# Performance work log

Measured on AMD Instinct MI355X. Metric: run time of the kernel, lower is better.

Reference implementation:

```python
import jax, jax.numpy as jnp
import numpy as np
from jax import lax

EPS = 1e-20
BN_EPS = 1e-5
ATTN_SCALE = 2.8284271247461903  # sqrt(d_l=8)
NS = (32, 32, 32, 10)
DS = (8, 8, 8, 16)


def squash(x):
    # Efficient-CapsNet squash: (1 - 1/(exp(||x||)+eps)) * x/(||x||+eps)
    norm = jnp.linalg.norm(x, axis=-1, keepdims=True)
    return (1.0 - 1.0 / (jnp.exp(norm) + EPS)) * (x / (norm + EPS))


def conv2d(x, w, b, stride, groups=1):
    y = lax.conv_general_dilated(
        x, w, window_strides=(stride, stride), padding='VALID',
        dimension_numbers=('NCHW', 'OIHW', 'NCHW'),
        feature_group_count=groups)
    return y + b[None, :, None, None]


def bn(x, g, b, m, v):
    inv = g / jnp.sqrt(v + BN_EPS)
    return x * inv[None, :, None, None] + (b - m * inv)[None, :, None, None]


def fccaps(U_l, W):
    # U_l: (b, n_l, d_l), W: (n_l, n_h, d_l, d_h)
    U_hat = jnp.einsum('bij,ikjl->bikl', U_l, W)          # (b, n_l, n_h, d_h)
    A = jnp.einsum('bikl,bhkl->bhik', U_hat, U_hat)        # (b, n_l, n_l, n_h)
    A_sum = jnp.sum(A, axis=-2)                            # (b, n_l, n_h)
    C = jax.nn.softmax(A_sum / ATTN_SCALE, axis=-1)        # (b, n_l, n_h)
    U_h = jnp.einsum('bikl,bik->bkl', U_hat, C)            # (b, n_h, d_h)
    return squash(U_h)


def setup_inputs() -> dict:
    key = jax.random.key(0)
    ks = jax.random.split(key, 8)
    B = 512
    x = jax.random.normal(ks[0], (B, 1, 39, 39), dtype=jnp.float32)
    conv1_w = jax.random.normal(ks[1], (128, 1, 3, 3), jnp.float32) * 0.2
    conv1_b = jnp.zeros((128,), jnp.float32)
    conv2_w = jax.random.normal(ks[2], (256, 128, 3, 3), jnp.float32) * 0.04
    conv2_b = jnp.zeros((256,), jnp.float32)
    conv3_w = jax.random.normal(ks[3], (256, 1, 9, 9), jnp.float32) * 0.1  # depthwise
    conv3_b = jnp.zeros((256,), jnp.float32)
    bn1_g = jnp.ones((128,), jnp.float32); bn1_b = jnp.zeros((128,), jnp.float32)
    bn1_m = jnp.zeros((128,), jnp.float32); bn1_v = jnp.ones((128,), jnp.float32)
    bn2_g = jnp.ones((256,), jnp.float32); bn2_b = jnp.zeros((256,), jnp.float32)
    bn2_m = jnp.zeros((256,), jnp.float32); bn2_v = jnp.ones((256,), jnp.float32)
    # capsule weights, kaiming-ish scale sqrt(2/fan_in) with fan_in = n_h*d_l*d_h
    def caps_w(k, n_l, n_h, d_l, d_h):
        std = np.sqrt(2.0 / (n_h * d_l * d_h))
        return jax.random.normal(k, (n_l, n_h, d_l, d_h), jnp.float32) * std
    W1 = caps_w(ks[4], NS[0], NS[1], DS[0], DS[1])
    W2 = caps_w(ks[5], NS[1], NS[2], DS[1], DS[2])
    W3 = caps_w(ks[6], NS[2], NS[3], DS[2], DS[3])
    return dict(x=x, conv1_w=conv1_w, conv1_b=conv1_b,
                bn1_g=bn1_g, bn1_b=bn1_b, bn1_m=bn1_m, bn1_v=bn1_v,
                conv2_w=conv2_w, conv2_b=conv2_b,
                bn2_g=bn2_g, bn2_b=bn2_b, bn2_m=bn2_m, bn2_v=bn2_v,
                conv3_w=conv3_w, conv3_b=conv3_b, W1=W1, W2=W2, W3=W3)


def reference(x, conv1_w, conv1_b, bn1_g, bn1_b, bn1_m, bn1_v,
              conv2_w, conv2_b, bn2_g, bn2_b, bn2_m, bn2_v,
              conv3_w, conv3_b, W1, W2, W3):
    h = jax.nn.relu(bn(conv2d(x, conv1_w, conv1_b, 2), bn1_g, bn1_b, bn1_m, bn1_v))
    h = jax.nn.relu(bn(conv2d(h, conv2_w, conv2_b, 2), bn2_g, bn2_b, bn2_m, bn2_v))
    h = conv2d(h, conv3_w, conv3_b, 1, groups=256)        # (B, 256, 1, 1)
    u = h.reshape(h.shape[0], NS[0], DS[0])                # (B, 32, 8)
    u = squash(u)
    for W in (W1, W2, W3):
        u = fccaps(u, W)
    return u  # (B, 10, 16)
```

## Files before the change

kernel.cpp:

```cpp
#include <hip/hip_runtime.h>


typedef __attribute__((ext_vector_type(8))) short short8;
typedef __attribute__((ext_vector_type(4))) float f32x4;

__device__ __forceinline__ ushort f2bf(float x) {
    uint u = __float_as_uint(x);
    return (ushort)((u + 0x7FFFu + ((u >> 16) & 1u)) >> 16);
}
__device__ __forceinline__ void bfsplit(float x, ushort& h, ushort& l) {
    h = f2bf(x);
    float hf = __uint_as_float(((uint)h) << 16);
    l = f2bf(x - hf);
}

__global__ __launch_bounds__(256) void k_prep(
    const float* __restrict__ w2, uint* __restrict__ Bt,
    const float* __restrict__ w3, float* __restrict__ w3T,
    const float* __restrict__ W1, const float* __restrict__ W2,
    const float* __restrict__ W3, float* __restrict__ Wr1,
    float* __restrict__ Wr2, float* __restrict__ Wr3,
    const float* __restrict__ c1b, const float* __restrict__ g1,
    const float* __restrict__ b1, const float* __restrict__ m1,
    const float* __restrict__ v1, float2* __restrict__ sc1) {
    __shared__ __align__(16) float wbuf[64 * 288];
    const int b = blockIdx.x, t = threadIdx.x;
    if (b < 144) {
        const int sidx = b >> 2, coq = b & 3;
        const int chunk = sidx / 9, tap = sidx - chunk * 9;
        const int co0 = coq * 64;
        for (int idx = t; idx < 4608; idx += 256) {
            const int n = idx / 72, q = idx - n * 72;
            ((float4*)wbuf)[n * 72 + q] =
                *(const float4*)(w2 + (size_t)(co0 + n) * 1152 + chunk * 288 + q * 4);
        }
        __syncthreads();
        const int n = t & 63, dg = (t >> 6) * 4;
        const int cot = coq >> 1, nn = ((coq & 1) * 64) + n;
        uint* dst = Bt + (size_t)(sidx * 2 + cot) * 4096;
#pragma unroll
        for (int dd = 0; dd < 4; ++dd) {
            const int d = dg + dd;
            const float x = wbuf[n * 288 + (2 * d) * 9 + tap];
            const float y = wbuf[n * 288 + (2 * d + 1) * 9 + tap];
            ushort xh, xl, yh, yl;
            bfsplit(x, xh, xl);
            bfsplit(y, yh, yl);
            dst[nn * 16 + d]        = (uint)xh | ((uint)yh << 16);
            dst[2048 + nn * 16 + d] = (uint)xl | ((uint)yl << 16);
        }
    } else if (b < 225) {
        const int p = b - 144;
        w3T[p * 256 + t] = w3[t * 81 + p];
    } else if (b < 321) {
        const int bb = b - 225;
        const int layer = bb >> 5, blk = bb & 31;
        const float* src = layer == 0 ? W1 : (layer == 1 ? W2 : W3);
        float* dst = layer == 0 ? Wr1 : (layer == 1 ? Wr2 : Wr3);
        const int d_h = (layer == 2) ? 16 : 8;
        const int total = (layer == 2) ? 5120 : 8192;
        for (int idx = blk * 256 + t; idx < 8 * total; idx += 32 * 256) {
            const int j = idx / total, e = idx - j * total;
            const int ik = e / d_h, l = e - ik * d_h;
            dst[idx] = src[(ik * 8 + j) * d_h + l];
        }
    } else {
        if (t < 128) {
            const float inv = g1[t] * rsqrtf(v1[t] + 1e-5f);
            sc1[t] = make_float2(inv, c1b[t] * inv + b1[t] - m1[t] * inv);
        }
    }
}

__global__ __launch_bounds__(512, 4) void k_conv2(
    const float* __restrict__ x, const float* __restrict__ w1,
    const float2* __restrict__ sc1, const uint* __restrict__ Bt,
    const float* __restrict__ g,
    const float* __restrict__ bb, const float* __restrict__ bm,
    const float* __restrict__ bv, const float* __restrict__ bias,
    const float* __restrict__ w3T, float* __restrict__ Uws) {
    __shared__ __align__(16) uint raw[11552];
    __shared__ __align__(16) float xs[1560];
    __shared__ float ured[256];
    const int t = threadIdx.x;
    const int lane = t & 63, wave = t >> 6;
    const int ln15 = lane & 15, lq = lane >> 4;
    const int wm = (wave >> 2) * 48;
    const int wn = (wave & 3) * 64;
    const int cot_w = (wave & 3) >> 1;
    const int bi = blockIdx.x;

    const float* xb = x + (size_t)bi * 1521;
    for (int i = t; i < 1521; i += 512) {
        const int y = i / 39, xc = i - y * 39;
        xs[y * 40 + xc] = xb[i];
    }

    const int qc = t & 15, ol = qc >> 2, qo = (qc & 3) * 2, pg = t >> 4;

    int PE[3], PO[3];
#pragma unroll
    for (int i = 0; i < 3; ++i) {
        const int m = wm + i * 16 + ln15;
        const int p = m < 81 ? m : 80;
        const int oh = p / 9, ow = p - oh * 9;
        PE[i] = lq * 760 + oh * 80 + ow * 4;
        PO[i] = 3040 + lq * 684 + oh * 72 + ow * 4;
    }
    int BRDg[4];
#pragma unroll
    for (int j = 0; j < 4; ++j) {
        const int n = ((wn & 64) + j * 16 + ln15);
        BRDg[j] = n * 16 + lq * 4;
    }

    f32x4 acc[3][4] = {};

#pragma unroll
    for (int c = 0; c < 4; ++c) {
        const int o_g = c * 32 + qc * 2;
        float wr[18];
        {
            const float2* wp = reinterpret_cast<const float2*>(w1 + o_g * 9);
#pragma unroll
            for (int q = 0; q < 9; ++q) {
                const float2 wv = wp[q];
                wr[q * 2] = wv.x; wr[q * 2 + 1] = wv.y;
            }
        }
        float2 ssv[2];
        ssv[0] = sc1[o_g];
        ssv[1] = sc1[o_g + 1];

        __syncthreads();

        {
            ushort* rawu = (ushort*)raw;
            for (int p = pg; p < 361; p += 32) {
                const int y = p / 19, xq = p - y * 19;
                const int b2 = y * 80 + xq * 2;
                const float2 x01 = *(const float2*)(xs + b2);
                const float  x2v = xs[b2 + 2];
                const float2 x34 = *(const float2*)(xs + b2 + 40);
                const float  x5v = xs[b2 + 42];
                const float2 x67 = *(const float2*)(xs + b2 + 80);
                const float  x8v = xs[b2 + 82];
                uint hw, lw;
                {
                    uint hv[2], lv[2];
#pragma unroll
                    for (int jj = 0; jj < 2; ++jj) {
                        const float a = x01.x * wr[jj * 9 + 0] + x01.y * wr[jj * 9 + 1] +
                                        x2v   * wr[jj * 9 + 2] + x34.x * wr[jj * 9 + 3] +
                                        x34.y * wr[jj * 9 + 4] + x5v   * wr[jj * 9 + 5] +
                                        x67.x * wr[jj * 9 + 6] + x67.y * wr[jj * 9 + 7] +
                                        x8v   * wr[jj * 9 + 8];
                        const float v = fmaxf(fmaf(a, ssv[jj].x, ssv[jj].y), 0.0f);
                        const uint u = __float_as_uint(v);
                        hv[jj] = u >> 16;
                        const float d = v - __uint_as_float(u & 0xFFFF0000u);
                        lv[jj] = __float_as_uint(d) >> 16;
                    }
                    hw = hv[0] | (hv[1] << 16);
                    lw = lv[0] | (lv[1] << 16);
                }
                int ad;
                if ((xq & 1) == 0) {
                    ad = ol * 1520 + (y * 10 + (xq >> 1)) * 8 + qo;
                } else {
                    ad = 6080 + ol * 1368 + (y * 9 + (xq >> 1)) * 8 + qo;
                }
                *(uint*)(rawu + ad)         = hw;
                *(uint*)(rawu + 11552 + ad) = lw;
            }
        }
        __syncthreads();

#pragma unroll
        for (int tap = 0; tap < 9; ++tap) {
            const int s = c * 9 + tap;
            const int kh = tap / 3, kw = tap - kh * 3;
            const int odd = kw & 1;
            const int sE = kh * 40 + (kw >> 1) * 4;
            const int sO = kh * 36;
            short8 a_h[3], a_l[3];
#pragma unroll
            for (int i = 0; i < 3; ++i) {
                const int addr = odd ? (PO[i] + sO) : (PE[i] + sE);
                a_h[i] = *reinterpret_cast<const short8*>(raw + addr);
                a_l[i] = *reinterpret_cast<const short8*>(raw + addr + 5776);
            }
            const uint* bp = Bt + (size_t)(s * 2 + cot_w) * 4096;
#pragma unroll
            for (int jh = 0; jh < 2; ++jh) {
                uint4 Bc[4];
#pragma unroll
                for (int j2 = 0; j2 < 2; ++j2) {
                    Bc[j2]     = *(const uint4*)(bp + BRDg[jh * 2 + j2]);
                    Bc[2 + j2] = *(const uint4*)(bp + 2048 + BRDg[jh * 2 + j2]);
                }
                short8 bh[2], bl[2];
#pragma unroll
                for (int j2 = 0; j2 < 2; ++j2) {
                    bh[j2] = __builtin_bit_cast(short8, Bc[j2]);
                    bl[j2] = __builtin_bit_cast(short8, Bc[2 + j2]);
                }
#pragma unroll
                for (int i = 0; i < 3; ++i)
#pragma unroll
                    for (int j2 = 0; j2 < 2; ++j2)
                        acc[i][jh * 2 + j2] = __builtin_amdgcn_mfma_f32_16x16x32_bf16(
                            a_h[i], bh[j2], acc[i][jh * 2 + j2], 0, 0, 0);
#pragma unroll
                for (int i = 0; i < 3; ++i)
#pragma unroll
                    for (int j2 = 0; j2 < 2; ++j2)
                        acc[i][jh * 2 + j2] = __builtin_amdgcn_mfma_f32_16x16x32_bf16(
                            a_h[i], bl[j2], acc[i][jh * 2 + j2], 0, 0, 0);
#pragma unroll
                for (int i = 0; i < 3; ++i)
#pragma unroll
                    for (int j2 = 0; j2 < 2; ++j2)
                        acc[i][jh * 2 + j2] = __builtin_amdgcn_mfma_f32_16x16x32_bf16(
                            a_l[i], bh[j2], acc[i][jh * 2 + j2], 0, 0, 0);
            }
        }
    }

    float scj[4], shj[4];
#pragma unroll
    for (int j = 0; j < 4; ++j) {
        const int co = wn + j * 16 + ln15;
        const float inv = g[co] * rsqrtf(bv[co] + 1e-5f);
        scj[j] = inv;
        shj[j] = bias[co] * inv + bb[co] - bm[co] * inv;
    }
    float usum[4] = {0.f, 0.f, 0.f, 0.f};
#pragma unroll
    for (int i = 0; i < 3; ++i)
#pragma unroll
        for (int r = 0; r < 4; ++r) {
            const int m = wm + i * 16 + lq * 4 + r;
            if (m < 81) {
                const float* wrow = w3T + m * 256;
#pragma unroll
                for (int j = 0; j < 4; ++j) {
                    const int col = wn + j * 16 + ln15;
                    const float v = fmaxf(fmaf(acc[i][j][r], scj[j], shj[j]), 0.0f);
                    usum[j] = fmaf(v, wrow[col], usum[j]);
                }
            }
        }
#pragma unroll
    for (int j = 0; j < 4; ++j) {
        usum[j] += __shfl_xor(usum[j], 16);
        usum[j] += __shfl_xor(usum[j], 32);
    }
    if (lq == 0 && wm == 0) {
#pragma unroll
        for (int j = 0; j < 4; ++j) ured[wn + j * 16 + ln15] = usum[j];
    }
    __syncthreads();
    if (lq == 0 && wm == 48) {
#pragma unroll
        for (int j = 0; j < 4; ++j) {
            const int col = wn + j * 16 + ln15;
            Uws[(size_t)bi * 256 + col] = usum[j] + ured[col];
        }
    }
}

__device__ __forceinline__ void fccaps_block(
    const int n_l, const int n_h, const int d_h, const float* __restrict__ Wr,
    float* U, float* Uh, float* Sv, float* Av, float* Cv, float* coefs,
    float* outU, const int t) {
    const int nkd = n_h * d_h;
    const int total = n_l * nkd;
    __syncthreads();
    for (int e = t; e < total; e += 256) {
        const int i = e / nkd;
        const float* up = U + i * 8;
        float acc = 0.0f;
#pragma unroll
        for (int j = 0; j < 8; ++j) acc += up[j] * Wr[j * total + e];
        Uh[e] = acc;
    }
    __syncthreads();
    for (int e = t; e < nkd; e += 256) {
        float acc = 0.0f;
        for (int i = 0; i < n_l; ++i) acc += Uh[i * nkd + e];
        Sv[e] = acc;
    }
    __syncthreads();
    for (int e = t; e < n_l * n_h; e += 256) {
        const int h = e / n_h, k = e - h * n_h;
        float acc = 0.0f;
        for (int l = 0; l < d_h; ++l)
            acc += Uh[h * nkd + k * d_h + l] * Sv[k * d_h + l];
        Av[e] = acc;
    }
    __syncthreads();
    {
        const int h = t >> 3, sub = t & 7;
        const float invs = 1.0f / 2.8284271247461903f;
        float mx = -1e30f;
        for (int k = sub; k < n_h; k += 8) mx = fmaxf(mx, Av[h * n_h + k]);
        mx = fmaxf(mx, __shfl_xor(mx, 1));
        mx = fmaxf(mx, __shfl_xor(mx, 2));
        mx = fmaxf(mx, __shfl_xor(mx, 4));
        float sum = 0.0f;
        for (int k = sub; k < n_h; k += 8) {
            const float ev = expf((Av[h * n_h + k] - mx) * invs);
            Cv[h * n_h + k] = ev;
            sum += ev;
        }
        sum += __shfl_xor(sum, 1);
        sum += __shfl_xor(sum, 2);
        sum += __shfl_xor(sum, 4);
        const float r = 1.0f / sum;
        for (int k = sub; k < n_h; k += 8) Cv[h * n_h + k] *= r;
    }
    __syncthreads();
    for (int e = t; e < nkd; e += 256) {
        const int k = e / d_h;
        float acc = 0.0f;
        for (int i = 0; i < n_l; ++i) acc += Uh[i * nkd + e] * Cv[i * n_h + k];
        Sv[e] = acc;
    }
    __syncthreads();
    if (t < n_h) {
        float ssq = 0.0f;
        for (int l = 0; l < d_h; ++l) { const float uv = Sv[t * d_h + l]; ssq += uv * uv; }
        const float n = sqrtf(ssq);
        coefs[t] = (1.0f - 1.0f / (expf(n) + 1e-20f)) / (n + 1e-20f);
    }
    __syncthreads();
    for (int e = t; e < nkd; e += 256) outU[e] = Sv[e] * coefs[e / d_h];
}

__global__ __launch_bounds__(256) void k_caps(
    const float* __restrict__ Uws, const float* __restrict__ b3,
    const float* __restrict__ Wr1, const float* __restrict__ Wr2,
    const float* __restrict__ Wr3, float* __restrict__ out) {
    __shared__ float U[256];
    __shared__ float Uh[8192];
    __shared__ float Sv[256];
    __shared__ float Av[1024];
    __shared__ float Cv[1024];
    __shared__ float coefs[32];
    const int b = blockIdx.x, t = threadIdx.x;
    U[t] = Uws[(size_t)b * 256 + t] + b3[t];
    __syncthreads();
    if (t < 32) {
        float ssq = 0.0f;
        for (int j = 0; j < 8; ++j) { const float uv = U[t * 8 + j]; ssq += uv * uv; }
        const float n = sqrtf(ssq);
        coefs[t] = (1.0f - 1.0f / (expf(n) + 1e-20f)) / (n + 1e-20f);
    }
    __syncthreads();
    U[t] *= coefs[t >> 3];
    fccaps_block(32, 32,  8, Wr1, U, Uh, Sv, Av, Cv, coefs, U, t);
    fccaps_block(32, 32,  8, Wr2, U, Uh, Sv, Av, Cv, coefs, U, t);
    fccaps_block(32, 10, 16, Wr3, U, Uh, Sv, Av, Cv, coefs, out + (size_t)b * 160, t);
}

extern "C" void kernel_launch(void* const* d_in, const int* in_sizes, int n_in,
                              void* d_out, int out_size, void* d_ws, size_t ws_size,
                              hipStream_t stream) {
    const float* x    = (const float*)d_in[0];
    const float* c1w  = (const float*)d_in[1];
    const float* c1b  = (const float*)d_in[2];
    const float* bn1g = (const float*)d_in[3];
    const float* bn1b = (const float*)d_in[4];
    const float* bn1m = (const float*)d_in[5];
    const float* bn1v = (const float*)d_in[6];
    const float* c2w  = (const float*)d_in[7];
    const float* c2b  = (const float*)d_in[8];
    const float* bn2g = (const float*)d_in[9];
    const float* bn2b = (const float*)d_in[10];
    const float* bn2m = (const float*)d_in[11];
    const float* bn2v = (const float*)d_in[12];
    const float* c3w  = (const float*)d_in[13];
    const float* c3b  = (const float*)d_in[14];
    const float* W1   = (const float*)d_in[15];
    const float* W2   = (const float*)d_in[16];
    const float* W3   = (const float*)d_in[17];
    float* out = (float*)d_out;
    uint*  wsu = (uint*)d_ws;
    float* wsf = (float*)d_ws;

    float*  Uws = wsf;
    uint*   Bt  = wsu + 131072;
    float*  w3T = wsf + 425984;
    float*  Wr1 = wsf + 446720;
    float*  Wr2 = wsf + 512256;
    float*  Wr3 = wsf + 577792;
    float2* sc1 = (float2*)(wsf + 618752);

    k_prep<<<dim3(322), 256, 0, stream>>>(c2w, Bt, c3w, w3T, W1, W2, W3,
                                          Wr1, Wr2, Wr3,
                                          c1b, bn1g, bn1b, bn1m, bn1v, sc1);
    k_conv2<<<dim3(512), 512, 0, stream>>>(x, c1w, sc1, Bt,
                                           bn2g, bn2b, bn2m, bn2v,
                                           c2b, w3T, Uws);
    k_caps<<<dim3(512), 256, 0, stream>>>(Uws, c3b, Wr1, Wr2, Wr3, out);
}
```

Before: 202.3 us.

## Fuse capsule routing layers into conv kernel epilogue with vectorized weight layout

The separate capsule kernel is removed, and the three fully-connected capsule layers now run at the end of the conv kernel, reusing its shared-memory buffer. This drops one kernel launch and the global round trip of the per-sample 256-float capsule input. The prep kernel now lays out the capsule weights with the 8 input-dim values contiguous, so each output element loads them as two float4 reads. The cost is a longer conv kernel tail that runs while the convolution hardware work sits idle, and 512-thread blocks doing routing that has only about 256 elements of parallelism per stage.

```diff
diff --git a/kernel.cpp b/kernel.cpp
--- a/kernel.cpp
+++ b/kernel.cpp
@@ -60,7 +60,7 @@
         const int d_h = (layer == 2) ? 16 : 8;
         const int total = (layer == 2) ? 5120 : 8192;
         for (int idx = blk * 256 + t; idx < 8 * total; idx += 32 * 256) {
-            const int j = idx / total, e = idx - j * total;
+            const int e = idx >> 3, j = idx & 7;
             const int ik = e / d_h, l = e - ik * d_h;
             dst[idx] = src[(ik * 8 + j) * d_h + l];
         }
@@ -70,6 +70,77 @@
             sc1[t] = make_float2(inv, c1b[t] * inv + b1[t] - m1[t] * inv);
         }
     }
+}
+
+__device__ __forceinline__ void fccaps512(
+    const int n_l, const int n_h, const int d_h, const float* __restrict__ Wr,
+    float* U, float* Uh, float* Sv, float* Av, float* Cv, float* coefs,
+    float* outU, const int t) {
+    const int nkd = n_h * d_h;
+    const int total = n_l * nkd;
+    __syncthreads();
+    for (int e = t; e < total; e += 512) {
+        const int i = e / nkd;
+        const float4* w4 = (const float4*)(Wr + (size_t)e * 8);
+        const float4 wa = w4[0], wb = w4[1];
+        const float4* u4 = (const float4*)(U + i * 8);
+        const float4 ua = u4[0], ub = u4[1];
+        Uh[e] = ua.x * wa.x + ua.y * wa.y + ua.z * wa.z + ua.w * wa.w +
+                ub.x * wb.x + ub.y * wb.y + ub.z * wb.z + ub.w * wb.w;
+    }
+    __syncthreads();
+    for (int e = t; e < nkd; e += 512) {
+        float acc = 0.0f;
+        for (int i = 0; i < n_l; ++i) acc += Uh[i * nkd + e];
+        Sv[e] = acc;
+    }
+    __syncthreads();
+    for (int e = t; e < n_l * n_h; e += 512) {
+        const int h = e / n_h, k = e - h * n_h;
+        float acc = 0.0f;
+        for (int l = 0; l < d_h; ++l)
+            acc += Uh[h * nkd + k * d_h + l] * Sv[k * d_h + l];
+        Av[e] = acc;
+    }
+    __syncthreads();
+    {
+        const int h = t >> 3, sub = t & 7;
+        if (h < n_l) {
+            const float invs = 1.0f / 2.8284271247461903f;
+            float mx = -1e30f;
+            for (int k = sub; k < n_h; k += 8) mx = fmaxf(mx, Av[h * n_h + k]);
+            mx = fmaxf(mx, __shfl_xor(mx, 1));
+            mx = fmaxf(mx, __shfl_xor(mx, 2));
+            mx = fmaxf(mx, __shfl_xor(mx, 4));
+            float sum = 0.0f;
+            for (int k = sub; k < n_h; k += 8) {
+                const float ev = expf((Av[h * n_h + k] - mx) * invs);
+                Cv[h * n_h + k] = ev;
+                sum += ev;
+            }
+            sum += __shfl_xor(sum, 1);
+            sum += __shfl_xor(sum, 2);
+            sum += __shfl_xor(sum, 4);
+            const float r = 1.0f / sum;
+            for (int k = sub; k < n_h; k += 8) Cv[h * n_h + k] *= r;
+        }
+    }
+    __syncthreads();
+    for (int e = t; e < nkd; e += 512) {
+        const int k = e / d_h;
+        float acc = 0.0f;
+        for (int i = 0; i < n_l; ++i) acc += Uh[i * nkd + e] * Cv[i * n_h + k];
+        Sv[e] = acc;
+    }
+    __syncthreads();
+    if (t < n_h) {
+        float ssq = 0.0f;
+        for (int l = 0; l < d_h; ++l) { const float uv = Sv[t * d_h + l]; ssq += uv * uv; }
+        const float n = sqrtf(ssq);
+        coefs[t] = (1.0f - 1.0f / (expf(n) + 1e-20f)) / (n + 1e-20f);
+    }
+    __syncthreads();
+    for (int e = t; e < nkd; e += 512) outU[e] = Sv[e] * coefs[e / d_h];
 }
 
 __global__ __launch_bounds__(512, 4) void k_conv2(
@@ -78,7 +149,9 @@
     const float* __restrict__ g,
     const float* __restrict__ bb, const float* __restrict__ bm,
     const float* __restrict__ bv, const float* __restrict__ bias,
-    const float* __restrict__ w3T, float* __restrict__ Uws) {
+    const float* __restrict__ w3T, const float* __restrict__ b3,
+    const float* __restrict__ Wr1, const float* __restrict__ Wr2,
+    const float* __restrict__ Wr3, float* __restrict__ out) {
     __shared__ __align__(16) uint raw[11552];
     __shared__ __align__(16) float xs[1560];
     __shared__ float ured[256];
@@ -261,107 +334,34 @@
         for (int j = 0; j < 4; ++j) ured[wn + j * 16 + ln15] = usum[j];
     }
     __syncthreads();
+
+    float* cF    = (float*)raw;
+    float* Uh    = cF + 256;
+    float* Sv    = cF + 8448;
+    float* Av    = cF + 8704;
+    float* Cv    = cF + 9728;
+    float* coefs = cF + 10752;
+
     if (lq == 0 && wm == 48) {
 #pragma unroll
         for (int j = 0; j < 4; ++j) {
             const int col = wn + j * 16 + ln15;
-            Uws[(size_t)bi * 256 + col] = usum[j] + ured[col];
-        }
-    }
-}
-
-__device__ __forceinline__ void fccaps_block(
-    const int n_l, const int n_h, const int d_h, const float* __restrict__ Wr,
-    float* U, float* Uh, float* Sv, float* Av, float* Cv, float* coefs,
-    float* outU, const int t) {
-    const int nkd = n_h * d_h;
-    const int total = n_l * nkd;
-    __syncthreads();
-    for (int e = t; e < total; e += 256) {
-        const int i = e / nkd;
-        const float* up = U + i * 8;
-        float acc = 0.0f;
-#pragma unroll
-        for (int j = 0; j < 8; ++j) acc += up[j] * Wr[j * total + e];
-        Uh[e] = acc;
-    }
-    __syncthreads();
-    for (int e = t; e < nkd; e += 256) {
-        float acc = 0.0f;
-        for (int i = 0; i < n_l; ++i) acc += Uh[i * nkd + e];
-        Sv[e] = acc;
-    }
-    __syncthreads();
-    for (int e = t; e < n_l * n_h; e += 256) {
-        const int h = e / n_h, k = e - h * n_h;
-        float acc = 0.0f;
-        for (int l = 0; l < d_h; ++l)
-            acc += Uh[h * nkd + k * d_h + l] * Sv[k * d_h + l];
-        Av[e] = acc;
-    }
-    __syncthreads();
-    {
-        const int h = t >> 3, sub = t & 7;
-        const float invs = 1.0f / 2.8284271247461903f;
-        float mx = -1e30f;
-        for (int k = sub; k < n_h; k += 8) mx = fmaxf(mx, Av[h * n_h + k]);
-        mx = fmaxf(mx, __shfl_xor(mx, 1));
-        mx = fmaxf(mx, __shfl_xor(mx, 2));
-        mx = fmaxf(mx, __shfl_xor(mx, 4));
-        float sum = 0.0f;
-        for (int k = sub; k < n_h; k += 8) {
-            const float ev = expf((Av[h * n_h + k] - mx) * invs);
-            Cv[h * n_h + k] = ev;
-            sum += ev;
-        }
-        sum += __shfl_xor(sum, 1);
-        sum += __shfl_xor(sum, 2);
-        sum += __shfl_xor(sum, 4);
-        const float r = 1.0f / sum;
-        for (int k = sub; k < n_h; k += 8) Cv[h * n_h + k] *= r;
-    }
-    __syncthreads();
-    for (int e = t; e < nkd; e += 256) {
-        const int k = e / d_h;
-        float acc = 0.0f;
-        for (int i = 0; i < n_l; ++i) acc += Uh[i * nkd + e] * Cv[i * n_h + k];
-        Sv[e] = acc;
-    }
-    __syncthreads();
-    if (t < n_h) {
+            cF[col] = usum[j] + ured[col] + b3[col];
+        }
+    }
+    __syncthreads();
+    if (t < 32) {
         float ssq = 0.0f;
-        for (int l = 0; l < d_h; ++l) { const float uv = Sv[t * d_h + l]; ssq += uv * uv; }
+        for (int j = 0; j < 8; ++j) { const float uv = cF[t * 8 + j]; ssq += uv * uv; }
         const float n = sqrtf(ssq);
         coefs[t] = (1.0f - 1.0f / (expf(n) + 1e-20f)) / (n + 1e-20f);
     }
     __syncthreads();
-    for (int e = t; e < nkd; e += 256) outU[e] = Sv[e] * coefs[e / d_h];
-}
-
-__global__ __launch_bounds__(256) void k_caps(
-    const float* __restrict__ Uws, const float* __restrict__ b3,
-    const float* __restrict__ Wr1, const float* __restrict__ Wr2,
-    const float* __restrict__ Wr3, float* __restrict__ out) {
-    __shared__ float U[256];
-    __shared__ float Uh[8192];
-    __shared__ float Sv[256];
-    __shared__ float Av[1024];
-    __shared__ float Cv[1024];
-    __shared__ float coefs[32];
-    const int b = blockIdx.x, t = threadIdx.x;
-    U[t] = Uws[(size_t)b * 256 + t] + b3[t];
-    __syncthreads();
-    if (t < 32) {
-        float ssq = 0.0f;
-        for (int j = 0; j < 8; ++j) { const float uv = U[t * 8 + j]; ssq += uv * uv; }
-        const float n = sqrtf(ssq);
-        coefs[t] = (1.0f - 1.0f / (expf(n) + 1e-20f)) / (n + 1e-20f);
-    }
-    __syncthreads();
-    U[t] *= coefs[t >> 3];
-    fccaps_block(32, 32,  8, Wr1, U, Uh, Sv, Av, Cv, coefs, U, t);
-    fccaps_block(32, 32,  8, Wr2, U, Uh, Sv, Av, Cv, coefs, U, t);
-    fccaps_block(32, 10, 16, Wr3, U, Uh, Sv, Av, Cv, coefs, out + (size_t)b * 160, t);
+    if (t < 256) cF[t] *= coefs[t >> 3];
+
+    fccaps512(32, 32,  8, Wr1, cF, Uh, Sv, Av, Cv, coefs, cF, t);
+    fccaps512(32, 32,  8, Wr2, cF, Uh, Sv, Av, Cv, coefs, cF, t);
+    fccaps512(32, 10, 16, Wr3, cF, Uh, Sv, Av, Cv, coefs, out + (size_t)bi * 160, t);
 }
 
 extern "C" void kernel_launch(void* const* d_in, const int* in_sizes, int n_in,
@@ -389,7 +389,6 @@
     uint*  wsu = (uint*)d_ws;
     float* wsf = (float*)d_ws;
 
-    float*  Uws = wsf;
     uint*   Bt  = wsu + 131072;
     float*  w3T = wsf + 425984;
     float*  Wr1 = wsf + 446720;
@@ -402,6 +401,5 @@
                                           c1b, bn1g, bn1b, bn1m, bn1v, sc1);
     k_conv2<<<dim3(512), 512, 0, stream>>>(x, c1w, sc1, Bt,
                                            bn2g, bn2b, bn2m, bn2v,
-                                           c2b, w3T, Uws);
-    k_caps<<<dim3(512), 256, 0, stream>>>(Uws, c3b, Wr1, Wr2, Wr3, out);
-}
+                                           c2b, w3T, c3b, Wr1, Wr2, Wr3, out);
+}
```

After: 196.7 us. 1.03x faster.
